# Kernel tuning notes

Hardware: AMD Instinct MI355X
Metric: run time of the kernel (lower is better)

## Reference

```python
import jax, jax.numpy as jnp
import numpy as np

B, T, DU, DM, DA, DF = 8, 2048, 512, 512, 256, 12
L_STAGES = 4   # number of routing stages
R_ITERS = 1    # diversity refinement iterations in selector
GAMMA = 1.0    # coverage_gamma
EPS = 1e-6
SCALE = float(np.sqrt(DA))


def setup_inputs() -> dict:
    key = jax.random.key(0)
    ks = jax.random.split(key, 16)
    w = lambda k, shape, fan_in: (jax.random.normal(k, shape, jnp.float32) / np.sqrt(fan_in)).astype(jnp.float32)
    return {
        'u': jax.random.normal(ks[0], (B, T, DU), jnp.float32),
        'structural_features': jax.random.normal(ks[1], (B, T, DF), jnp.float32),
        'similarity': jax.random.uniform(ks[2], (B, T, T), jnp.float32),
        'memory0': jax.random.normal(ks[3], (B, DM), jnp.float32),
        'Wq': w(ks[4], (DA, DM), DM),
        'Wk': w(ks[5], (DA, DU), DU),
        'Wv': w(ks[6], (DU, DU), DU),
        'sb_w1': w(ks[7], (DA, 3), 3),
        'sb_b1': jnp.zeros((DA,), jnp.float32),
        'sb_w2': w(ks[8], (1, DA), DA),
        'sb_b2': jnp.zeros((1,), jnp.float32),
        'log_temp': jnp.zeros((), jnp.float32),
        'W_ih': w(ks[9], (3 * DM, DU + 4), DU + 4),
        'b_ih': jnp.zeros((3 * DM,), jnp.float32),
        'W_hh': w(ks[10], (3 * DM, DM), DM),
        'b_hh': jnp.zeros((3 * DM,), jnp.float32),
    }


def _selection_stats(y, u):
    # y: [B,T], u: [B,T,DU] -> c: [B,4]
    Tn = u.shape[1]
    y_sum = jnp.maximum(y.sum(axis=1), EPS)                      # [B]
    coverage = y.sum(axis=1) / Tn
    y_norm = y / y_sum[:, None]
    entropy = -(y_norm * jnp.log(jnp.maximum(y_norm, EPS))).sum(axis=1)
    centroid = jnp.einsum('bt,btd->bd', y, u)                    # unnormalized [B,DU]
    cen = centroid / y_sum[:, None]
    dist = jnp.linalg.norm(u - cen[:, None, :], axis=-1)         # [B,T]
    spread = (y * dist).sum(axis=1) / y_sum
    wsq = (y * jnp.sum(u * u, axis=-1)).sum(axis=1)              # [B]
    csq = jnp.sum(centroid * centroid, axis=1)
    compact = 2.0 * (y_sum * wsq - csq) / jnp.maximum(y_sum * y_sum, EPS)
    return jnp.stack([coverage, entropy, spread, compact], axis=1)


def reference(u, structural_features, similarity, memory0, Wq, Wk, Wv,
              sb_w1, sb_b1, sb_w2, sb_b2, log_temp, W_ih, b_ih, W_hh, b_hh):
    k = jnp.einsum('btu,au->bta', u, Wk)                         # [B,T,DA]
    v = jnp.einsum('btu,vu->btv', u, Wv)                         # [B,T,DU]
    desc = structural_features[..., -4:-1]                       # [B,T,3]
    sbias = (jax.nn.gelu(desc @ sb_w1.T + sb_b1, approximate=False) @ sb_w2.T + sb_b2)[..., 0]
    temp = jnp.clip(jnp.exp(log_temp), 0.1, 10.0)
    memory = memory0
    prev = None
    outs = []
    for _ in range(L_STAGES):
        q = memory @ Wq.T                                        # [B,DA]
        scores = jnp.einsum('bta,ba->bt', k, q) / SCALE + sbias
        if prev is not None:
            scores = scores - GAMMA * jnp.einsum('bts,bs->bt', similarity, prev)
        logits = scores / temp
        y = jax.nn.softmax(logits, axis=1)
        for _r in range(R_ITERS):
            overlap = jnp.einsum('bts,bs->bt', similarity, y)
            penalty = overlap / jnp.maximum(jnp.max(overlap, axis=1, keepdims=True), EPS)
            logits = logits - penalty
            y = jax.nn.softmax(logits, axis=1)
        z = jnp.einsum('bt,btd->bd', y, v)                       # stage token [B,DU]
        c = _selection_stats(y, u)                               # [B,4]
        x = jnp.concatenate([z, c], axis=-1)
        gi = x @ W_ih.T + b_ih
        gh = memory @ W_hh.T + b_hh
        gir, giz, gin = jnp.split(gi, 3, axis=-1)
        ghr, ghz, ghn = jnp.split(gh, 3, axis=-1)
        rg = jax.nn.sigmoid(gir + ghr)
        zg = jax.nn.sigmoid(giz + ghz)
        ng = jnp.tanh(gin + rg * ghn)
        memory = (1.0 - zg) * ng + zg * memory                   # GRUCell update
        prev = y if prev is None else prev + y
        outs.append(z)
    return jnp.stack(outs, axis=1)                               # [B,L,DU]
```

## Files before the change

kernel.cpp:

```cpp
#include <hip/hip_runtime.h>
#include <math.h>

constexpr int cB = 8, cT = 2048, cDU = 512, cDM = 512, cDA = 256, cDF = 12, cL = 4;
constexpr float cEPS = 1e-6f;
constexpr float cSCALE = 16.0f;
constexpr float cGAMMA = 1.0f;

typedef unsigned short u16;
typedef unsigned char u8;
typedef u16 u16x8 __attribute__((ext_vector_type(8)));

constexpr size_t F_SB = 0;
constexpr size_t F_UN = F_SB + 16384;
constexpr size_t F_LG = F_UN + 16384;
constexpr size_t F_Y  = F_LG + 16384;
constexpr size_t F_PR = F_Y  + 16384;
constexpr size_t F_OV = F_PR + 16384;
constexpr size_t F_SP = F_OV + 16384;
constexpr size_t F_QK = F_SP + 256;
constexpr size_t F_M0 = F_QK + 4096;
constexpr size_t F_M1 = F_M0 + 4096;
constexpr size_t F_C  = F_M1 + 4096;
constexpr size_t F_Z  = F_C  + 4096;
constexpr size_t F_SC = F_Z  + 4096;
constexpr size_t F_A  = F_SC + 64;
constexpr size_t F_END = F_A + 262144;
constexpr size_t U_OFFB   = F_END * 4;
constexpr size_t U_BYTES  = (size_t)cB * cT * cDU * 2;
constexpr size_t S8_OFFB  = U_OFFB + U_BYTES;
constexpr size_t S8_BYTES = (size_t)cB * cT * cT;
constexpr size_t WS_NEED_U   = S8_OFFB;
constexpr size_t WS_NEED_ALL = S8_OFFB + S8_BYTES;

__device__ __forceinline__ float wave_sum(float v) {
#pragma unroll
  for (int o = 32; o; o >>= 1) v += __shfl_down(v, o);
  return v;
}
__device__ __forceinline__ u16 f2bf(float f) {
  unsigned u = __float_as_uint(f);
  return (u16)((u + 0x7fffu + ((u >> 16) & 1u)) >> 16);
}
__device__ __forceinline__ float bf2f(u16 h) { return __uint_as_float(((unsigned)h) << 16); }
__device__ __forceinline__ float dot4(float4 a, float4 b) {
  return a.x * b.x + a.y * b.y + a.z * b.z + a.w * b.w;
}
__device__ __forceinline__ unsigned pack4(float a, float b, float c, float d) {
  unsigned b0 = (unsigned)(a * 255.f + 0.5f);
  unsigned b1 = (unsigned)(b * 255.f + 0.5f);
  unsigned b2 = (unsigned)(c * 255.f + 0.5f);
  unsigned b3 = (unsigned)(d * 255.f + 0.5f);
  return b0 | (b1 << 8) | (b2 << 16) | (b3 << 24);
}
__device__ __forceinline__ void dotu8(float& sd, unsigned w, float4 p) {
  sd += (float)(w & 255u) * p.x + (float)((w >> 8) & 255u) * p.y +
        (float)((w >> 16) & 255u) * p.z + (float)(w >> 24) * p.w;
}

__global__ __launch_bounds__(256) void k_init(
    const float* __restrict__ u, const float* __restrict__ sf,
    const float* __restrict__ mem0,
    const float* __restrict__ Wq, const float* __restrict__ Wk,
    const float* __restrict__ w1, const float* __restrict__ b1,
    const float* __restrict__ w2, const float* __restrict__ b2,
    float* __restrict__ wsf, u16* __restrict__ ubf, int use_ubf) {
  const int tid = threadIdx.x;
  if (blockIdx.x >= 1024) {
    __shared__ float wkj[32][8];
    int j0 = (blockIdx.x - 1024) * 8;
    float acc[8][2] = {};
    for (int a0 = 0; a0 < cDA; a0 += 32) {
      wkj[tid >> 3][tid & 7] = Wk[(size_t)(a0 + (tid >> 3)) * cDU + j0 + (tid & 7)];
      __syncthreads();
#pragma unroll 8
      for (int aa = 0; aa < 32; ++aa) {
        float wq0 = Wq[(size_t)(a0 + aa) * cDM + tid * 2];
        float wq1 = Wq[(size_t)(a0 + aa) * cDM + tid * 2 + 1];
#pragma unroll
        for (int r = 0; r < 8; ++r) {
          acc[r][0] += wkj[aa][r] * wq0;
          acc[r][1] += wkj[aa][r] * wq1;
        }
      }
      __syncthreads();
    }
#pragma unroll
    for (int r = 0; r < 8; ++r) {
      wsf[F_A + (size_t)(j0 + r) * cDU + tid * 2] = acc[r][0];
      wsf[F_A + (size_t)(j0 + r) * cDU + tid * 2 + 1] = acc[r][1];
    }
    return;
  }
  const int gt = blockIdx.x * 256 + tid;
  const int nt = 1024 * 256;
  const int wv = tid >> 6, lane = tid & 63;
  const int gw = blockIdx.x * 4 + wv;
  const int nw = 1024 * 4;

  for (int i = gt; i < cB * cDM; i += nt) wsf[F_M0 + i] = mem0[i];

  if (use_ubf) {
    const int NU8 = cB * cT * cDU / 8;
    const float4* src = (const float4*)u;
    for (int c = gt; c < NU8; c += nt) {
      float4 f0 = src[(size_t)c * 2], f1 = src[(size_t)c * 2 + 1];
      u16x8 o;
      o[0] = f2bf(f0.x); o[1] = f2bf(f0.y); o[2] = f2bf(f0.z); o[3] = f2bf(f0.w);
      o[4] = f2bf(f1.x); o[5] = f2bf(f1.y); o[6] = f2bf(f1.z); o[7] = f2bf(f1.w);
      *(u16x8*)(ubf + (size_t)c * 8) = o;
    }
  }
  for (int row = gw; row < cB * cT; row += nw) {
    float d0 = sf[(size_t)row * cDF + 8];
    float d1 = sf[(size_t)row * cDF + 9];
    float d2 = sf[(size_t)row * cDF + 10];
    float acc = 0.f;
#pragma unroll
    for (int i = 0; i < 4; ++i) {
      int a = lane * 4 + i;
      float h = d0 * w1[a * 3 + 0] + d1 * w1[a * 3 + 1] + d2 * w1[a * 3 + 2] + b1[a];
      float g = 0.5f * h * (1.0f + erff(h * 0.70710678118654752f));
      acc += g * w2[a];
    }
    float un = 0.f;
    const float4* ur = (const float4*)(u + (size_t)row * cDU);
#pragma unroll
    for (int m = 0; m < 2; ++m) { float4 x = ur[lane + m * 64]; un += dot4(x, x); }
    acc = wave_sum(acc);
    un = wave_sum(un);
    if (lane == 0) { wsf[F_SB + row] = acc + b2[0]; wsf[F_UN + row] = un; }
  }
}

__global__ __launch_bounds__(256) void k_qk(const float* __restrict__ A,
                                            const float* __restrict__ mem,
                                            float* __restrict__ qk,
                                            float* __restrict__ c_raw) {
  int wv = threadIdx.x >> 6, lane = threadIdx.x & 63;
  int b = blockIdx.x & 7;
  int j = (blockIdx.x >> 3) * 4 + wv;
  const float4* ar = (const float4*)(A + (size_t)j * cDM);
  const float4* mr = (const float4*)(mem + (size_t)b * cDM);
  float acc = dot4(ar[lane * 2], mr[lane * 2]) + dot4(ar[lane * 2 + 1], mr[lane * 2 + 1]);
  acc = wave_sum(acc);
  if (lane == 0) qk[b * cDU + j] = acc;
  int gt = blockIdx.x * 256 + threadIdx.x;
  if (gt < cB * cDU) c_raw[gt] = 0.f;
}

__global__ __launch_bounds__(256) void k_scores(
    const u16* __restrict__ ubf, const float* __restrict__ uf,
    const float* __restrict__ qk, const float* __restrict__ sbias,
    const u8* __restrict__ sim8, const float* __restrict__ simf,
    const float* __restrict__ prev, const float* __restrict__ log_temp,
    float gamma, int use_ubf, int use_s8, float* __restrict__ logits) {
  int wv = threadIdx.x >> 6;
  int lane = threadIdx.x & 63;
  int b = blockIdx.x & 7;
  int t = (blockIdx.x >> 3) * 4 + wv;
  int grow = b * cT + t;
  const float4* qk4 = (const float4*)(qk + (size_t)b * cDU);
  float4 q0 = qk4[lane * 2], q1 = qk4[lane * 2 + 1];
  float acc;
  if (use_ubf) {
    u16x8 s = *(const u16x8*)(ubf + (size_t)grow * cDU + lane * 8);
    acc = bf2f(s[0]) * q0.x + bf2f(s[1]) * q0.y + bf2f(s[2]) * q0.z + bf2f(s[3]) * q0.w +
          bf2f(s[4]) * q1.x + bf2f(s[5]) * q1.y + bf2f(s[6]) * q1.z + bf2f(s[7]) * q1.w;
  } else {
    const float4* ur = (const float4*)(uf + (size_t)grow * cDU);
    acc = dot4(ur[lane * 2], q0) + dot4(ur[lane * 2 + 1], q1);
  }
  acc *= (1.0f / cSCALE);
  if (gamma != 0.0f) {
    float sd = 0.f;
    const float4* pr4 = (const float4*)(prev + (size_t)b * cT);
    if (use_s8) {
#pragma unroll
      for (int m = 0; m < 2; ++m) {
        uint4 sq = *(const uint4*)(sim8 + (size_t)grow * cT + m * 1024 + lane * 16);
        const float4* pb = pr4 + m * 256 + lane * 4;
        dotu8(sd, sq.x, pb[0]); dotu8(sd, sq.y, pb[1]);
        dotu8(sd, sq.z, pb[2]); dotu8(sd, sq.w, pb[3]);
      }
      sd *= (1.0f / 255.0f);
    } else {
      const float4* sr = (const float4*)(simf + (size_t)grow * cT);
#pragma unroll
      for (int m = 0; m < 8; ++m) sd += dot4(sr[lane + m * 64], pr4[lane + m * 64]);
    }
    acc -= gamma * sd;
  }
  acc = wave_sum(acc);
  if (lane == 0) {
    float temp = fminf(fmaxf(expf(log_temp[0]), 0.1f), 10.0f);
    logits[grow] = (acc + sbias[grow]) / temp;
  }
}

__global__ __launch_bounds__(256) void k_overlap(
    const u8* __restrict__ sim8c, u8* __restrict__ sim8w,
    const float* __restrict__ simf,
    const float* __restrict__ logits, int use_s8, int convert,
    float* __restrict__ overlap) {
  __shared__ float ylds[2176];
  __shared__ float red[256];
  const int tid = threadIdx.x;
  const int wv = tid >> 6, lane = tid & 63;
  const int b = blockIdx.x & 7;
  const int ch = blockIdx.x >> 3;
  float l[8];
  float mx = -INFINITY;
#pragma unroll
  for (int e = 0; e < 8; ++e) { l[e] = logits[b * cT + e * 256 + tid]; mx = fmaxf(mx, l[e]); }
  red[tid] = mx; __syncthreads();
  for (int s2 = 128; s2; s2 >>= 1) { if (tid < s2) red[tid] = fmaxf(red[tid], red[tid + s2]); __syncthreads(); }
  mx = red[0]; __syncthreads();
  float sum = 0.f;
#pragma unroll
  for (int e = 0; e < 8; ++e) {
    float ev = expf(l[e] - mx);
    sum += ev;
    int s = e * 256 + tid;
    ylds[s + (s >> 4)] = ev;
  }
  red[tid] = sum; __syncthreads();
  for (int s2 = 128; s2; s2 >>= 1) { if (tid < s2) red[tid] += red[tid + s2]; __syncthreads(); }
  float invS = 1.f / red[0];
  __syncthreads();
  for (int r = 0; r < 4; ++r) {
    int row = b * cT + ch * 16 + wv * 4 + r;
    float acc = 0.f;
    if (use_s8 && !convert) {
#pragma unroll
      for (int m = 0; m < 2; ++m) {
        uint4 sq = *(const uint4*)(sim8c + (size_t)row * cT + m * 1024 + lane * 16);
        int s0 = m * 1024 + lane * 16;
#pragma unroll
        for (int k = 0; k < 4; ++k) {
          unsigned w = (&sq.x)[k];
          int s = s0 + k * 4;
          acc += (float)(w & 255u)         * ylds[s + (s >> 4)] +
                 (float)((w >> 8) & 255u)  * ylds[(s + 1) + ((s + 1) >> 4)] +
                 (float)((w >> 16) & 255u) * ylds[(s + 2) + ((s + 2) >> 4)] +
                 (float)(w >> 24)          * ylds[(s + 3) + ((s + 3) >> 4)];
        }
      }
      acc *= (1.0f / 255.0f);
    } else {
#pragma unroll
      for (int m = 0; m < 2; ++m) {
        const float4* sr = (const float4*)(simf + (size_t)row * cT + m * 1024 + lane * 16);
        uint4 oq;
#pragma unroll
        for (int k = 0; k < 4; ++k) {
          float4 sv = sr[k];
          int s = m * 1024 + lane * 16 + k * 4;
          acc += sv.x * ylds[s + (s >> 4)] + sv.y * ylds[(s + 1) + ((s + 1) >> 4)] +
                 sv.z * ylds[(s + 2) + ((s + 2) >> 4)] + sv.w * ylds[(s + 3) + ((s + 3) >> 4)];
          (&oq.x)[k] = pack4(sv.x, sv.y, sv.z, sv.w);
        }
        if (convert)
          *(uint4*)(sim8w + (size_t)row * cT + m * 1024 + lane * 16) = oq;
      }
    }
    acc = wave_sum(acc);
    if (lane == 0) overlap[row] = acc * invS;
  }
}

__global__ __launch_bounds__(256) void k_statcen(
    const float* __restrict__ overlap, const float* __restrict__ logits,
    const float* __restrict__ unorm2,
    const u16* __restrict__ ubf, const float* __restrict__ uf, int use_ubf,
    float* __restrict__ y, float* __restrict__ prev,
    float* __restrict__ scal, float* __restrict__ c_raw, int first_stage) {
  __shared__ float ylds[2048];
  __shared__ float comb[2048];
  __shared__ float red[256];
  const int tid = threadIdx.x;
  const int wv = tid >> 6, lane = tid & 63;
  const int b = blockIdx.x & 7;
  const int ch = blockIdx.x >> 3;
  float o[8], l[8], yv[8];
  float mo = -INFINITY;
#pragma unroll
  for (int e = 0; e < 8; ++e) { o[e] = overlap[b * cT + e * 256 + tid]; mo = fmaxf(mo, o[e]); }
  red[tid] = mo; __syncthreads();
  for (int s2 = 128; s2; s2 >>= 1) { if (tid < s2) red[tid] = fmaxf(red[tid], red[tid + s2]); __syncthreads(); }
  mo = fmaxf(red[0], cEPS); __syncthreads();
  float ml = -INFINITY;
#pragma unroll
  for (int e = 0; e < 8; ++e) { l[e] = logits[b * cT + e * 256 + tid] - o[e] / mo; ml = fmaxf(ml, l[e]); }
  red[tid] = ml; __syncthreads();
  for (int s2 = 128; s2; s2 >>= 1) { if (tid < s2) red[tid] = fmaxf(red[tid], red[tid + s2]); __syncthreads(); }
  ml = red[0]; __syncthreads();
  float sum = 0.f;
#pragma unroll
  for (int e = 0; e < 8; ++e) { l[e] = expf(l[e] - ml); sum += l[e]; }
  red[tid] = sum; __syncthreads();
  for (int s2 = 128; s2; s2 >>= 1) { if (tid < s2) red[tid] += red[tid + s2]; __syncthreads(); }
  float inv = 1.f / red[0]; __syncthreads();
  float ysr_p = 0.f, wsq_p = 0.f;
#pragma unroll
  for (int e = 0; e < 8; ++e) {
    yv[e] = l[e] * inv;
    ylds[e * 256 + tid] = yv[e];
    ysr_p += yv[e];
    wsq_p += yv[e] * unorm2[b * cT + e * 256 + tid];
  }
  red[tid] = ysr_p; __syncthreads();
  for (int s2 = 128; s2; s2 >>= 1) { if (tid < s2) red[tid] += red[tid + s2]; __syncthreads(); }
  float ysr = red[0]; __syncthreads();
  float ysc = fmaxf(ysr, cEPS);
  red[tid] = wsq_p; __syncthreads();
  for (int s2 = 128; s2; s2 >>= 1) { if (tid < s2) red[tid] += red[tid + s2]; __syncthreads(); }
  float wsq = red[0]; __syncthreads();
  float ent_p = 0.f;
#pragma unroll
  for (int e = 0; e < 8; ++e) {
    float yn = yv[e] / ysc;
    ent_p -= yn * logf(fmaxf(yn, cEPS));
  }
  red[tid] = ent_p; __syncthreads();
  for (int s2 = 128; s2; s2 >>= 1) { if (tid < s2) red[tid] += red[tid + s2]; __syncthreads(); }
  float ent = red[0]; __syncthreads();
  if (ch == 0) {
#pragma unroll
    for (int e = 0; e < 8; ++e) {
      int idx = b * cT + e * 256 + tid;
      y[idx] = yv[e];
      if (first_stage) prev[idx] = yv[e]; else prev[idx] += yv[e];
    }
    if (tid == 0) {
      scal[b * 8 + 0] = ysc;
      scal[b * 8 + 1] = ysr / (float)cT;
      scal[b * 8 + 2] = ent;
      scal[b * 8 + 3] = wsq;
    }
  }
  float acc[8] = {};
  for (int i = 0; i < 16; ++i) {
    int r = ch * 64 + wv * 16 + i;
    float yvv = ylds[r];
    int row = b * cT + r;
    if (use_ubf) {
      u16x8 s8 = *(const u16x8*)(ubf + (size_t)row * cDU + lane * 8);
#pragma unroll
      for (int e = 0; e < 8; ++e) acc[e] += yvv * bf2f(s8[e]);
    } else {
      const float4* ur = (const float4*)(uf + (size_t)row * cDU);
      float4 a0 = ur[lane * 2], a1 = ur[lane * 2 + 1];
      acc[0] += yvv * a0.x; acc[1] += yvv * a0.y; acc[2] += yvv * a0.z; acc[3] += yvv * a0.w;
      acc[4] += yvv * a1.x; acc[5] += yvv * a1.y; acc[6] += yvv * a1.z; acc[7] += yvv * a1.w;
    }
  }
  __syncthreads();
#pragma unroll
  for (int e = 0; e < 8; ++e) comb[wv * 512 + lane * 8 + e] = acc[e];
  __syncthreads();
  float s0 = comb[tid] + comb[512 + tid] + comb[1024 + tid] + comb[1536 + tid];
  float s1 = comb[tid + 256] + comb[512 + tid + 256] + comb[1024 + tid + 256] + comb[1536 + tid + 256];
  atomicAdd(&c_raw[b * cDU + tid], s0);
  atomicAdd(&c_raw[b * cDU + tid + 256], s1);
}

__global__ __launch_bounds__(256) void k_zyd(
    const float* __restrict__ c_raw, const float* __restrict__ Wv,
    const u16* __restrict__ ubf, const float* __restrict__ uf, int use_ubf,
    const float* __restrict__ unorm2, const float* __restrict__ y,
    float* __restrict__ z, float* __restrict__ scal, float* __restrict__ sprp) {
  __shared__ float s4[4];
  int wv = threadIdx.x >> 6, lane = threadIdx.x & 63;
  if (blockIdx.x < 1024) {
    int b = blockIdx.x & 7;
    int j = (blockIdx.x >> 3) * 4 + wv;
    const float4* c4 = (const float4*)(c_raw + (size_t)b * cDU);
    const float4* w4 = (const float4*)(Wv + (size_t)j * cDU);
    float acc = dot4(c4[lane * 2], w4[lane * 2]) + dot4(c4[lane * 2 + 1], w4[lane * 2 + 1]);
    acc = wave_sum(acc);
    if (lane == 0) z[b * cDU + j] = acc;
    return;
  }
  int unit = blockIdx.x - 1024;
  int b = unit & 7, tc = unit >> 3;
  float ysc = scal[b * 8 + 0];
  float inv = 1.f / ysc;
  const float4* c4 = (const float4*)(c_raw + (size_t)b * cDU);
  float4 cr0 = c4[lane * 2], cr1 = c4[lane * 2 + 1];
  float4 cx0, cx1;
  cx0.x = cr0.x * inv; cx0.y = cr0.y * inv; cx0.z = cr0.z * inv; cx0.w = cr0.w * inv;
  cx1.x = cr1.x * inv; cx1.y = cr1.y * inv; cx1.z = cr1.z * inv; cx1.w = cr1.w * inv;
  float cen2 = wave_sum(dot4(cx0, cx0) + dot4(cx1, cx1));
  if (tc == 0 && wv == 0) {
    float csq = wave_sum(dot4(cr0, cr0) + dot4(cr1, cr1));
    if (lane == 0) scal[b * 8 + 6] = csq;
  }
  float part = 0.f;
  for (int i = 0; i < 16; ++i) {
    int row = b * cT + tc * 64 + wv * 16 + i;
    float dot;
    if (use_ubf) {
      u16x8 s = *(const u16x8*)(ubf + (size_t)row * cDU + lane * 8);
      dot = bf2f(s[0]) * cx0.x + bf2f(s[1]) * cx0.y + bf2f(s[2]) * cx0.z + bf2f(s[3]) * cx0.w +
            bf2f(s[4]) * cx1.x + bf2f(s[5]) * cx1.y + bf2f(s[6]) * cx1.z + bf2f(s[7]) * cx1.w;
    } else {
      const float4* ur = (const float4*)(uf + (size_t)row * cDU);
      dot = dot4(ur[lane * 2], cx0) + dot4(ur[lane * 2 + 1], cx1);
    }
    dot = wave_sum(dot);
    if (lane == 0) {
      float d2 = unorm2[row] - 2.f * dot + cen2;
      part += y[row] * sqrtf(fmaxf(d2, 0.f));
    }
  }
  if (lane == 0) s4[wv] = part;
  __syncthreads();
  if (threadIdx.x == 0) sprp[b * 32 + tc] = s4[0] + s4[1] + s4[2] + s4[3];
}

__global__ __launch_bounds__(256) void k_gru(const float* __restrict__ z,
                                             const float* __restrict__ scal,
                                             const float* __restrict__ sprp,
                                             const float* __restrict__ memin,
                                             float* __restrict__ memout,
                                             const float* __restrict__ W_ih,
                                             const float* __restrict__ b_ih,
                                             const float* __restrict__ W_hh,
                                             const float* __restrict__ b_hh,
                                             float* __restrict__ out, int stage) {
  int wid = blockIdx.x * 4 + (threadIdx.x >> 6);
  int lane = threadIdx.x & 63;
  int b = wid >> 9, i = wid & 511;
  const float4* xz = (const float4*)(z + (size_t)b * cDU);
  const float4* xm = (const float4*)(memin + (size_t)b * cDM);
  float4 z0 = xz[lane * 2], z1 = xz[lane * 2 + 1];
  float4 m0 = xm[lane * 2], m1 = xm[lane * 2 + 1];
  float ysc = scal[b * 8 + 0];
  float sv = (lane < 32) ? sprp[b * 32 + lane] : 0.f;
  float spr_raw = wave_sum(sv);
  float aI[3], aH[3];
#pragma unroll
  for (int g = 0; g < 3; ++g) {
    size_t row = (size_t)(g * 512 + i);
    const float4* wI = (const float4*)(W_ih + row * 516);
    float a = dot4(z0, wI[lane * 2]) + dot4(z1, wI[lane * 2 + 1]);
    if (lane == 0) {
      float4 wt = wI[128];
      float cov = scal[b * 8 + 1], ent = scal[b * 8 + 2];
      float spr = spr_raw / ysc;
      float cmp = 2.f * (ysc * scal[b * 8 + 3] - scal[b * 8 + 6]) / fmaxf(ysc * ysc, cEPS);
      a += cov * wt.x + ent * wt.y + spr * wt.z + cmp * wt.w;
    }
    aI[g] = wave_sum(a);
    const float4* wH = (const float4*)(W_hh + row * cDM);
    float h = dot4(m0, wH[lane * 2]) + dot4(m1, wH[lane * 2 + 1]);
    aH[g] = wave_sum(h);
  }
  if (lane == 0) {
    float gir = aI[0] + b_ih[i],        ghr = aH[0] + b_hh[i];
    float giz = aI[1] + b_ih[512 + i],  ghz = aH[1] + b_hh[512 + i];
    float gin = aI[2] + b_ih[1024 + i], ghn = aH[2] + b_hh[1024 + i];
    float rg = 1.f / (1.f + expf(-(gir + ghr)));
    float zg = 1.f / (1.f + expf(-(giz + ghz)));
    float ng = tanhf(gin + rg * ghn);
    float mold = memin[b * cDM + i];
    memout[b * cDM + i] = (1.f - zg) * ng + zg * mold;
    out[(size_t)(b * cL + stage) * cDU + i] = z[b * cDU + i];
  }
}

extern "C" void kernel_launch(void* const* d_in, const int* in_sizes, int n_in,
                              void* d_out, int out_size, void* d_ws, size_t ws_size,
                              hipStream_t stream) {
  const float* u    = (const float*)d_in[0];
  const float* sf   = (const float*)d_in[1];
  const float* sim  = (const float*)d_in[2];
  const float* mem0 = (const float*)d_in[3];
  const float* Wq   = (const float*)d_in[4];
  const float* Wk   = (const float*)d_in[5];
  const float* Wv   = (const float*)d_in[6];
  const float* sbw1 = (const float*)d_in[7];
  const float* sbb1 = (const float*)d_in[8];
  const float* sbw2 = (const float*)d_in[9];
  const float* sbb2 = (const float*)d_in[10];
  const float* logt = (const float*)d_in[11];
  const float* W_ih = (const float*)d_in[12];
  const float* b_ih = (const float*)d_in[13];
  const float* W_hh = (const float*)d_in[14];
  const float* b_hh = (const float*)d_in[15];
  float* out = (float*)d_out;
  float* ws  = (float*)d_ws;
  u16* ubf  = (u16*)((char*)d_ws + U_OFFB);
  u8* sim8  = (u8*)((char*)d_ws + S8_OFFB);

  const int use_ubf = (ws_size >= WS_NEED_U) ? 1 : 0;
  const int use_s8  = (ws_size >= WS_NEED_ALL) ? 1 : 0;

  k_init<<<1088, 256, 0, stream>>>(u, sf, mem0, Wq, Wk, sbw1, sbb1, sbw2, sbb2,
                                   ws, ubf, use_ubf);

  for (int stage = 0; stage < cL; ++stage) {
    float* mcur = ws + ((stage & 1) ? F_M1 : F_M0);
    float* mnxt = ws + ((stage & 1) ? F_M0 : F_M1);
    k_qk<<<1024, 256, 0, stream>>>(ws + F_A, mcur, ws + F_QK, ws + F_C);
    k_scores<<<4096, 256, 0, stream>>>(ubf, u, ws + F_QK, ws + F_SB, sim8, sim,
                                       ws + F_PR, logt, stage == 0 ? 0.0f : cGAMMA,
                                       use_ubf, use_s8, ws + F_LG);
    k_overlap<<<1024, 256, 0, stream>>>(sim8, sim8, sim, ws + F_LG, use_s8,
                                        (stage == 0 && use_s8) ? 1 : 0, ws + F_OV);
    k_statcen<<<256, 256, 0, stream>>>(ws + F_OV, ws + F_LG, ws + F_UN,
                                       ubf, u, use_ubf,
                                       ws + F_Y, ws + F_PR, ws + F_SC, ws + F_C,
                                       stage == 0 ? 1 : 0);
    k_zyd<<<1280, 256, 0, stream>>>(ws + F_C, Wv, ubf, u, use_ubf,
                                    ws + F_UN, ws + F_Y, ws + F_Z, ws + F_SC, ws + F_SP);
    k_gru<<<1024, 256, 0, stream>>>(ws + F_Z, ws + F_SC, ws + F_SP, mcur, mnxt,
                                    W_ih, b_ih, W_hh, b_hh, out, stage);
  }
}
```

Measured before the change: 494.7 us.

## Rebalance work per block across scores, statcen and zyd kernels

k_scores now handles four rows per wave, loading the prev vector into registers once and reusing it, and launches a quarter as many blocks. k_statcen and k_zyd process fewer rows per block with more blocks (512 and 2048), so more waves run at once for these memory-bound passes, and the spread partial buffer grows from 32 to 128 entries per batch. The aim is to cut redundant prev loads in the scoring pass and raise parallelism in the small reduction kernels. The cost is more partial sums and atomic or centroid contributions in statcen, and fewer blocks in scores.

New measurement: 464.0 us. 1.07x faster.

```diff
diff --git a/kernel.cpp b/kernel.cpp
--- a/kernel.cpp
+++ b/kernel.cpp
@@ -17,7 +17,7 @@
 constexpr size_t F_PR = F_Y  + 16384;
 constexpr size_t F_OV = F_PR + 16384;
 constexpr size_t F_SP = F_OV + 16384;
-constexpr size_t F_QK = F_SP + 256;
+constexpr size_t F_QK = F_SP + 1024;
 constexpr size_t F_M0 = F_QK + 4096;
 constexpr size_t F_M1 = F_M0 + 4096;
 constexpr size_t F_C  = F_M1 + 4096;
@@ -157,43 +157,53 @@
   int wv = threadIdx.x >> 6;
   int lane = threadIdx.x & 63;
   int b = blockIdx.x & 7;
-  int t = (blockIdx.x >> 3) * 4 + wv;
-  int grow = b * cT + t;
+  int t0 = ((blockIdx.x >> 3) * 4 + wv) * 4;
   const float4* qk4 = (const float4*)(qk + (size_t)b * cDU);
   float4 q0 = qk4[lane * 2], q1 = qk4[lane * 2 + 1];
-  float acc;
-  if (use_ubf) {
-    u16x8 s = *(const u16x8*)(ubf + (size_t)grow * cDU + lane * 8);
-    acc = bf2f(s[0]) * q0.x + bf2f(s[1]) * q0.y + bf2f(s[2]) * q0.z + bf2f(s[3]) * q0.w +
-          bf2f(s[4]) * q1.x + bf2f(s[5]) * q1.y + bf2f(s[6]) * q1.z + bf2f(s[7]) * q1.w;
-  } else {
-    const float4* ur = (const float4*)(uf + (size_t)grow * cDU);
-    acc = dot4(ur[lane * 2], q0) + dot4(ur[lane * 2 + 1], q1);
-  }
-  acc *= (1.0f / cSCALE);
-  if (gamma != 0.0f) {
-    float sd = 0.f;
+  float4 pv[8];
+  const bool haveP = (gamma != 0.0f) && use_s8;
+  if (haveP) {
     const float4* pr4 = (const float4*)(prev + (size_t)b * cT);
-    if (use_s8) {
-#pragma unroll
-      for (int m = 0; m < 2; ++m) {
-        uint4 sq = *(const uint4*)(sim8 + (size_t)grow * cT + m * 1024 + lane * 16);
-        const float4* pb = pr4 + m * 256 + lane * 4;
-        dotu8(sd, sq.x, pb[0]); dotu8(sd, sq.y, pb[1]);
-        dotu8(sd, sq.z, pb[2]); dotu8(sd, sq.w, pb[3]);
+#pragma unroll
+    for (int m = 0; m < 2; ++m)
+#pragma unroll
+      for (int k = 0; k < 4; ++k) pv[m * 4 + k] = pr4[m * 256 + lane * 4 + k];
+  }
+  float temp = fminf(fmaxf(expf(log_temp[0]), 0.1f), 10.0f);
+#pragma unroll
+  for (int i = 0; i < 4; ++i) {
+    int grow = b * cT + t0 + i;
+    float acc;
+    if (use_ubf) {
+      u16x8 s = *(const u16x8*)(ubf + (size_t)grow * cDU + lane * 8);
+      acc = bf2f(s[0]) * q0.x + bf2f(s[1]) * q0.y + bf2f(s[2]) * q0.z + bf2f(s[3]) * q0.w +
+            bf2f(s[4]) * q1.x + bf2f(s[5]) * q1.y + bf2f(s[6]) * q1.z + bf2f(s[7]) * q1.w;
+    } else {
+      const float4* ur = (const float4*)(uf + (size_t)grow * cDU);
+      acc = dot4(ur[lane * 2], q0) + dot4(ur[lane * 2 + 1], q1);
+    }
+    acc *= (1.0f / cSCALE);
+    if (gamma != 0.0f) {
+      float sd = 0.f;
+      if (use_s8) {
+        const u8* sr = sim8 + (size_t)grow * cT;
+        uint4 sq0 = *(const uint4*)(sr + lane * 16);
+        uint4 sq1 = *(const uint4*)(sr + 1024 + lane * 16);
+        dotu8(sd, sq0.x, pv[0]); dotu8(sd, sq0.y, pv[1]);
+        dotu8(sd, sq0.z, pv[2]); dotu8(sd, sq0.w, pv[3]);
+        dotu8(sd, sq1.x, pv[4]); dotu8(sd, sq1.y, pv[5]);
+        dotu8(sd, sq1.z, pv[6]); dotu8(sd, sq1.w, pv[7]);
+        sd *= (1.0f / 255.0f);
+      } else {
+        const float4* sr = (const float4*)(simf + (size_t)grow * cT);
+        const float4* pr4 = (const float4*)(prev + (size_t)b * cT);
+#pragma unroll
+        for (int m = 0; m < 8; ++m) sd += dot4(sr[lane + m * 64], pr4[lane + m * 64]);
       }
-      sd *= (1.0f / 255.0f);
-    } else {
-      const float4* sr = (const float4*)(simf + (size_t)grow * cT);
-#pragma unroll
-      for (int m = 0; m < 8; ++m) sd += dot4(sr[lane + m * 64], pr4[lane + m * 64]);
-    }
-    acc -= gamma * sd;
-  }
-  acc = wave_sum(acc);
-  if (lane == 0) {
-    float temp = fminf(fmaxf(expf(log_temp[0]), 0.1f), 10.0f);
-    logits[grow] = (acc + sbias[grow]) / temp;
+      acc -= gamma * sd;
+    }
+    acc = wave_sum(acc);
+    if (lane == 0) logits[grow] = (acc + sbias[grow]) / temp;
   }
 }
 
@@ -339,8 +349,8 @@
     }
   }
   float acc[8] = {};
-  for (int i = 0; i < 16; ++i) {
-    int r = ch * 64 + wv * 16 + i;
+  for (int i = 0; i < 8; ++i) {
+    int r = ch * 32 + wv * 8 + i;
     float yvv = ylds[r];
     int row = b * cT + r;
     if (use_ubf) {
@@ -396,8 +406,8 @@
     if (lane == 0) scal[b * 8 + 6] = csq;
   }
   float part = 0.f;
-  for (int i = 0; i < 16; ++i) {
-    int row = b * cT + tc * 64 + wv * 16 + i;
+  for (int i = 0; i < 4; ++i) {
+    int row = b * cT + tc * 16 + wv * 4 + i;
     float dot;
     if (use_ubf) {
       u16x8 s = *(const u16x8*)(ubf + (size_t)row * cDU + lane * 8);
@@ -415,7 +425,7 @@
   }
   if (lane == 0) s4[wv] = part;
   __syncthreads();
-  if (threadIdx.x == 0) sprp[b * 32 + tc] = s4[0] + s4[1] + s4[2] + s4[3];
+  if (threadIdx.x == 0) sprp[b * 128 + tc] = s4[0] + s4[1] + s4[2] + s4[3];
 }
 
 __global__ __launch_bounds__(256) void k_gru(const float* __restrict__ z,
@@ -436,7 +446,7 @@
   float4 z0 = xz[lane * 2], z1 = xz[lane * 2 + 1];
   float4 m0 = xm[lane * 2], m1 = xm[lane * 2 + 1];
   float ysc = scal[b * 8 + 0];
-  float sv = (lane < 32) ? sprp[b * 32 + lane] : 0.f;
+  float sv = sprp[b * 128 + lane] + sprp[b * 128 + 64 + lane];
   float spr_raw = wave_sum(sv);
   float aI[3], aH[3];
 #pragma unroll
@@ -503,16 +513,16 @@
     float* mcur = ws + ((stage & 1) ? F_M1 : F_M0);
     float* mnxt = ws + ((stage & 1) ? F_M0 : F_M1);
     k_qk<<<1024, 256, 0, stream>>>(ws + F_A, mcur, ws + F_QK, ws + F_C);
-    k_scores<<<4096, 256, 0, stream>>>(ubf, u, ws + F_QK, ws + F_SB, sim8, sim,
+    k_scores<<<1024, 256, 0, stream>>>(ubf, u, ws + F_QK, ws + F_SB, sim8, sim,
                                        ws + F_PR, logt, stage == 0 ? 0.0f : cGAMMA,
                                        use_ubf, use_s8, ws + F_LG);
     k_overlap<<<1024, 256, 0, stream>>>(sim8, sim8, sim, ws + F_LG, use_s8,
                                         (stage == 0 && use_s8) ? 1 : 0, ws + F_OV);
-    k_statcen<<<256, 256, 0, stream>>>(ws + F_OV, ws + F_LG, ws + F_UN,
+    k_statcen<<<512, 256, 0, stream>>>(ws + F_OV, ws + F_LG, ws + F_UN,
                                        ubf, u, use_ubf,
                                        ws + F_Y, ws + F_PR, ws + F_SC, ws + F_C,
                                        stage == 0 ? 1 : 0);
-    k_zyd<<<1280, 256, 0, stream>>>(ws + F_C, Wv, ubf, u, use_ubf,
+    k_zyd<<<2048, 256, 0, stream>>>(ws + F_C, Wv, ubf, u, use_ubf,
                                     ws + F_UN, ws + F_Y, ws + F_Z, ws + F_SC, ws + F_SP);
     k_gru<<<1024, 256, 0, stream>>>(ws + F_Z, ws + F_SC, ws + F_SP, mcur, mnxt,
                                     W_ih, b_ih, W_hh, b_hh, out, stage);
```
